# Kernel optimization log

Hardware: AMD Instinct MI355X
Metric: run time of the kernel (lower is better)

## Reference

```python
import jax, jax.numpy as jnp
import numpy as np

NUM_HEADS = 12
PRUNE_THRESHOLD = 0.5  # deterministic stand-in for torch.rand(1).item() seed_


def setup_inputs() -> dict:
    key = jax.random.key(0)
    ks = jax.random.split(key, 7)
    B, f, w, W, D = 4, 16, 8, 128, 768
    Bn = B * f * w
    return {
        "x": jax.random.normal(ks[0], (Bn, W, D), dtype=jnp.float32),
        "qkv_w": jax.random.normal(ks[1], (3 * D, D), dtype=jnp.float32) * (D ** -0.5),
        "qkv_b": jax.random.normal(ks[2], (3 * D,), dtype=jnp.float32) * 0.01,
        "proj_w": jax.random.normal(ks[3], (D, D), dtype=jnp.float32) * (D ** -0.5),
        "proj_b": jax.random.normal(ks[4], (D,), dtype=jnp.float32) * 0.01,
        "edge_bias": jax.random.uniform(ks[5], (1, NUM_HEADS, W, W), dtype=jnp.float32),
        "mask": jax.random.uniform(ks[6], (f * w, W, W), dtype=jnp.float32),
        "B": B,
        "f": f,
        "w": w,
    }


def reference(x, qkv_w, qkv_b, proj_w, proj_b, edge_bias, mask, B, f, w):
    Bn, W, D = x.shape              # Bn = B*f*w windows, W = tokens per window
    H = NUM_HEADS
    hd = D // H
    scale = hd ** -0.5

    qkv = x @ qkv_w.T + qkv_b                                   # [Bn, W, 3D]
    qkv = qkv.reshape(Bn, W, 3, H, hd).transpose(2, 0, 3, 1, 4)  # [3, Bn, H, W, hd]
    q, k, v = qkv[0] * scale, qkv[1], qkv[2]

    attn = jnp.einsum('bhqd,bhkd->bhqk', q, k)                  # [Bn, H, W, W]

    # stochastic softmax-threshold pruning (training branch), detached mask
    probs = jax.nn.softmax(attn, axis=-1)
    keep = jnp.where(probs > PRUNE_THRESHOLD, 0.0, 1.0)
    attn = attn * jax.lax.stop_gradient(keep)

    attn5 = attn.reshape(B, f * w, H, W, W)
    attn5 = attn5 * mask[None, :, None, :, :]                   # mask: [f*w, W, W]
    attn5 = attn5 * edge_bias[:, None]                          # edge_bias: [1, H, W, W]
    attn = attn5.reshape(Bn, H, W, W)

    attn = jnp.where(attn == 0, jnp.float32(-10000.0), attn)
    attn = jax.nn.softmax(attn, axis=-1)

    out = jnp.einsum('bhqk,bhkd->bhqd', attn, v)                # [Bn, H, W, hd]
    out = out.transpose(0, 2, 1, 3).reshape(Bn, W, D)
    return out @ proj_w.T + proj_b
```

## Files before the change

kernel.cpp:

```cpp
#include <hip/hip_runtime.h>

#define NW 512
#define WT 128
#define DM 768
#define NH 12

typedef __attribute__((ext_vector_type(8))) short bf16x8;
typedef __attribute__((ext_vector_type(4))) float f32x4;
typedef __attribute__((ext_vector_type(4))) unsigned int u32x4;

#define W1CH 12288
#define WS_W1 ((size_t)NH * 24 * W1CH)
#define PWCHUNK 49152
#define WS_W2 ((size_t)24 * PWCHUNK)

__device__ __forceinline__ unsigned short bf_rne(float v) {
  unsigned u = __float_as_uint(v);
  unsigned r = u + 0x7fffu + ((u >> 16) & 1u);
  return (unsigned short)(r >> 16);
}
__device__ __forceinline__ void bf_split(float v, unsigned short& hi, unsigned short& lo) {
  hi = bf_rne(v);
  float hf = __uint_as_float(((unsigned)hi) << 16);
  lo = bf_rne(v - hf);
}

__device__ __forceinline__ unsigned cvt_pk_bf16(float a, float b) {
  unsigned r;
  asm("v_cvt_pk_bf16_f32 %0, %1, %2" : "=v"(r) : "v"(a), "v"(b));
  return r;
}
__device__ __forceinline__ unsigned short bf_rne_fast(float v) {
  return (unsigned short)cvt_pk_bf16(v, v);
}
__device__ __forceinline__ void bf_split_fast(float v, unsigned short& hi, unsigned short& lo) {
  unsigned hp = cvt_pk_bf16(v, v);
  float hf = __uint_as_float(hp << 16);
  lo = (unsigned short)cvt_pk_bf16(v - hf, v - hf);
  hi = (unsigned short)hp;
}

__device__ __forceinline__ void split8(float4 v0, float4 v1, bf16x8& hi, bf16x8& lo) {
  float f[8] = {v0.x, v0.y, v0.z, v0.w, v1.x, v1.y, v1.z, v1.w};
  u32x4 hu, lu;
#pragma unroll
  for (int i = 0; i < 4; ++i) {
    float e0 = f[2 * i], e1 = f[2 * i + 1];
    unsigned hp = cvt_pk_bf16(e0, e1);
    float h0 = __uint_as_float(hp << 16);
    float h1 = __uint_as_float(hp & 0xffff0000u);
    lu[i] = cvt_pk_bf16(e0 - h0, e1 - h1);
    hu[i] = hp;
  }
  hi = __builtin_bit_cast(bf16x8, hu);
  lo = __builtin_bit_cast(bf16x8, lu);
}

__device__ __forceinline__ void gl_lds16(const void* g, void* l) {
  __builtin_amdgcn_global_load_lds(
      (const __attribute__((address_space(1))) void*)g,
      (__attribute__((address_space(3))) void*)l, 16, 0, 0);
}

__global__ __launch_bounds__(256) void split_w_kernel(
    const float* __restrict__ qkv_w, unsigned char* __restrict__ wsW)
{
  int id = blockIdx.x * 256 + threadIdx.x;
  int c4 = id & 7;
  int j  = (id >> 3) % 192;
  int hc = (id >> 3) / 192;
  int c  = hc % 24;
  int h  = hc / 24;
  int sec = j >> 6, d = j & 63;
  const float* src = qkv_w + (size_t)(sec * DM + h * 64 + d) * DM + c * 32 + c4 * 4;
  float4 v = *(const float4*)src;
  uint2 hv;
  hv.x = (unsigned)bf_rne(v.x) | ((unsigned)bf_rne(v.y) << 16);
  hv.y = (unsigned)bf_rne(v.z) | ((unsigned)bf_rne(v.w) << 16);
  int byte = j * 64 + (((c4 >> 1) ^ ((j >> 1) & 3)) << 4) + ((c4 & 1) << 3);
  *(uint2*)(wsW + (size_t)hc * W1CH + byte) = hv;
}

__global__ __launch_bounds__(256) void split_pw_kernel(
    const float* __restrict__ pw, unsigned char* __restrict__ wsP)
{
  int id = blockIdx.x * 256 + threadIdx.x;
  int c4 = id & 7;
  int n  = (id >> 3) % 768;
  int c  = (id >> 3) / 768;
  float4 v = *(const float4*)(pw + (size_t)n * DM + c * 32 + c4 * 4);
  uint2 hv;
  hv.x = (unsigned)bf_rne(v.x) | ((unsigned)bf_rne(v.y) << 16);
  hv.y = (unsigned)bf_rne(v.z) | ((unsigned)bf_rne(v.w) << 16);
  int byte = n * 64 + (((c4 >> 1) ^ ((n >> 1) & 3)) << 4) + ((c4 & 1) << 3);
  *(uint2*)(wsP + (size_t)c * PWCHUNK + byte) = hv;
}

#define QH_OFF 0
#define QL_OFF 16384
#define KH_OFF 32768
#define KL_OFF 49152
#define VT_OFF 65536
#define EX_OFF 49152
#define P_OFF  0

__global__ __launch_bounds__(512, 4) void attn_kernel_pre(
    const float* __restrict__ x, const unsigned char* __restrict__ wimg,
    const float* __restrict__ qkv_b, const float* __restrict__ edge_bias,
    const float* __restrict__ mask, float* __restrict__ out)
{
  __shared__ __align__(16) unsigned char smem[81920];
  const int t = threadIdx.x;
  const int lane = t & 63;
  const int w = t >> 6;
  const int g = lane >> 4;
  const int ln = lane & 15;
  const int wm = w & 3;
  const int wn = w >> 2;

  const int orig = blockIdx.x;
  const int wg = (orig & 7) * 768 + (orig >> 3);
  const int h = wg % 12;
  const int bn = wg / 12;

  const float* xw = x + (size_t)bn * (WT * DM);
  const unsigned char* whead = wimg + (size_t)h * (24 * W1CH);

  f32x4 acc[2][6];
#pragma unroll
  for (int i = 0; i < 2; ++i)
#pragma unroll
    for (int j = 0; j < 6; ++j) acc[i][j] = (f32x4){0.f, 0.f, 0.f, 0.f};

  const int exr = wm * 32 + (lane & 31);
  const int exs = wn * 2 + (lane >> 5);
  const float* xptr = xw + (size_t)exr * DM + wn * 16 + (lane >> 5) * 8;
  const int ex_w_hi = exr * 128 + ((exs ^ (exr & 7)) << 4);
  const int ex_w_lo = exr * 128 + (((exs + 4) ^ (exr & 7)) << 4);
  int ex_r_h[2], ex_r_l[2];
#pragma unroll
  for (int sm = 0; sm < 2; ++sm) {
    int rr = wm * 32 + sm * 16 + ln;
    ex_r_h[sm] = rr * 128 + ((g ^ (rr & 7)) << 4);
    ex_r_l[sm] = rr * 128 + (((g + 4) ^ (rr & 7)) << 4);
  }

  {
    gl_lds16(whead + t * 16, smem + t * 16);
    if (t < 256) gl_lds16(whead + 8192 + t * 16, smem + 8192 + t * 16);
  }
  __builtin_amdgcn_sched_barrier(0);
  float4 xa = *(const float4*)xptr;
  float4 xb = *(const float4*)(xptr + 4);
  __builtin_amdgcn_sched_barrier(0);

  for (int c = 0; c < 24; ++c) {
    float4 na, nb;
    if (c < 23) {
      na = *(const float4*)(xptr + (c + 1) * 32);
      nb = *(const float4*)(xptr + (c + 1) * 32 + 4);
    }
    __builtin_amdgcn_sched_barrier(0);
    bf16x8 xh8, xl8;
    split8(xa, xb, xh8, xl8);
    unsigned char* exb = smem + EX_OFF + (c & 1) * 16384;
    *(bf16x8*)(exb + ex_w_hi) = xh8;
    *(bf16x8*)(exb + ex_w_lo) = xl8;
    __builtin_amdgcn_sched_barrier(0);
    if (c < 23) asm volatile("s_waitcnt vmcnt(2)" ::: "memory");
    else        asm volatile("s_waitcnt vmcnt(0)" ::: "memory");
    asm volatile("s_waitcnt lgkmcnt(0)" ::: "memory");
    __builtin_amdgcn_s_barrier();
    __builtin_amdgcn_sched_barrier(0);
    if (c < 23) {
      const unsigned char* src = whead + (size_t)(c + 1) * W1CH;
      unsigned char* dst = smem + ((c + 1) & 1) * W1CH;
      gl_lds16(src + t * 16, dst + t * 16);
      if (t < 256) gl_lds16(src + 8192 + t * 16, dst + 8192 + t * 16);
    }
    __builtin_amdgcn_sched_barrier(0);
    const unsigned char* WH = smem + (c & 1) * W1CH;
    bf16x8 ah0 = *(const bf16x8*)(exb + ex_r_h[0]);
    bf16x8 al0 = *(const bf16x8*)(exb + ex_r_l[0]);
    bf16x8 ah1 = *(const bf16x8*)(exb + ex_r_h[1]);
    bf16x8 al1 = *(const bf16x8*)(exb + ex_r_l[1]);
    __builtin_amdgcn_s_setprio(1);
#pragma unroll
    for (int ns = 0; ns < 6; ++ns) {
      int j = (ns * 2 + wn) * 16 + ln;
      int sw = j * 64 + ((g ^ ((j >> 1) & 3)) << 4);
      bf16x8 bh = *(const bf16x8*)(WH + sw);
      acc[0][ns] = __builtin_amdgcn_mfma_f32_16x16x32_bf16(ah0, bh, acc[0][ns], 0, 0, 0);
      acc[1][ns] = __builtin_amdgcn_mfma_f32_16x16x32_bf16(ah1, bh, acc[1][ns], 0, 0, 0);
      if (ns < 4) {
        acc[0][ns] = __builtin_amdgcn_mfma_f32_16x16x32_bf16(al0, bh, acc[0][ns], 0, 0, 0);
        acc[1][ns] = __builtin_amdgcn_mfma_f32_16x16x32_bf16(al1, bh, acc[1][ns], 0, 0, 0);
      }
    }
    __builtin_amdgcn_s_setprio(0);
    xa = na; xb = nb;
  }
  __syncthreads();

#pragma unroll
  for (int ns = 0; ns < 6; ++ns) {
    int cc = (ns * 2 + wn) * 16 + ln;
    int sec = cc >> 6, dd = cc & 63;
    float bias = qkv_b[sec * DM + h * 64 + dd];
#pragma unroll
    for (int sm = 0; sm < 2; ++sm) {
#pragma unroll
      for (int r = 0; r < 4; ++r) {
        int m = wm * 32 + sm * 16 + 4 * g + r;
        float val = acc[sm][ns][r] + bias;
        if (cc < 64) {
          val *= 0.125f;
          unsigned short hi, lo; bf_split_fast(val, hi, lo);
          int byte = m * 128 + (((dd >> 3) ^ (m & 7)) << 4) + ((dd & 7) << 1);
          *(unsigned short*)(smem + QH_OFF + byte) = hi;
          *(unsigned short*)(smem + QL_OFF + byte) = lo;
        } else if (cc < 128) {
          unsigned short hi, lo; bf_split_fast(val, hi, lo);
          int byte = m * 128 + (((dd >> 3) ^ (m & 7)) << 4) + ((dd & 7) << 1);
          *(unsigned short*)(smem + KH_OFF + byte) = hi;
          *(unsigned short*)(smem + KL_OFF + byte) = lo;
        } else {
          int byte = dd * 256 + ((((m >> 3) ^ (dd & 15))) << 4) + ((m & 7) << 1);
          *(unsigned short*)(smem + VT_OFF + byte) = bf_rne_fast(val);
        }
      }
    }
  }
  __syncthreads();

  const int mB = w * 16;
  f32x4 s2[8];
#pragma unroll
  for (int ns = 0; ns < 8; ++ns) s2[ns] = (f32x4){0.f, 0.f, 0.f, 0.f};
#pragma unroll
  for (int ks = 0; ks < 2; ++ks) {
    int arow = mB + ln;
    int abyte = arow * 128 + (((ks * 4 + g) ^ (arow & 7)) << 4);
    bf16x8 qh = *(const bf16x8*)(smem + QH_OFF + abyte);
    bf16x8 ql = *(const bf16x8*)(smem + QL_OFF + abyte);
#pragma unroll
    for (int ns = 0; ns < 8; ++ns) {
      int brow = ns * 16 + ln;
      int bbyte = brow * 128 + (((ks * 4 + g) ^ (brow & 7)) << 4);
      bf16x8 kh = *(const bf16x8*)(smem + KH_OFF + bbyte);
      bf16x8 kl = *(const bf16x8*)(smem + KL_OFF + bbyte);
      s2[ns] = __builtin_amdgcn_mfma_f32_16x16x32_bf16(qh, kh, s2[ns], 0, 0, 0);
      s2[ns] = __builtin_amdgcn_mfma_f32_16x16x32_bf16(qh, kl, s2[ns], 0, 0, 0);
      s2[ns] = __builtin_amdgcn_mfma_f32_16x16x32_bf16(ql, kh, s2[ns], 0, 0, 0);
    }
  }
  __syncthreads();

  const float* mk = mask + (size_t)(bn & 127) * (WT * WT);
  const float* eb = edge_bias + (size_t)h * (WT * WT);
#pragma unroll
  for (int r = 0; r < 4; ++r) {
    int m = mB + 4 * g + r;
    float sv[8];
#pragma unroll
    for (int ns = 0; ns < 8; ++ns) sv[ns] = s2[ns][r];
    float m1 = sv[0];
#pragma unroll
    for (int ns = 1; ns < 8; ++ns) m1 = fmaxf(m1, sv[ns]);
#pragma unroll
    for (int off = 1; off < 16; off <<= 1) m1 = fmaxf(m1, __shfl_xor(m1, off, 64));
    float e[8], sum1 = 0.f;
#pragma unroll
    for (int ns = 0; ns < 8; ++ns) { e[ns] = __expf(sv[ns] - m1); sum1 += e[ns]; }
#pragma unroll
    for (int off = 1; off < 16; off <<= 1) sum1 += __shfl_xor(sum1, off, 64);
    float thr = 0.5f * sum1;
    float tv[8];
#pragma unroll
    for (int ns = 0; ns < 8; ++ns) {
      int col = ns * 16 + ln;
      float mkv = mk[m * WT + col];
      float ebv = eb[m * WT + col];
      float keep = (e[ns] > thr) ? 0.f : 1.f;
      float val = sv[ns] * keep * mkv * ebv;
      tv[ns] = (val == 0.f) ? -10000.f : val;
    }
    float m2 = tv[0];
#pragma unroll
    for (int ns = 1; ns < 8; ++ns) m2 = fmaxf(m2, tv[ns]);
#pragma unroll
    for (int off = 1; off < 16; off <<= 1) m2 = fmaxf(m2, __shfl_xor(m2, off, 64));
    float e2[8], sum2 = 0.f;
#pragma unroll
    for (int ns = 0; ns < 8; ++ns) { e2[ns] = __expf(tv[ns] - m2); sum2 += e2[ns]; }
#pragma unroll
    for (int off = 1; off < 16; off <<= 1) sum2 += __shfl_xor(sum2, off, 64);
    float inv = 1.f / sum2;
#pragma unroll
    for (int ns = 0; ns < 8; ++ns)
      *(unsigned short*)(smem + P_OFF + m * 272 + (ns * 16 + ln) * 2) = bf_rne_fast(e2[ns] * inv);
  }
  __syncthreads();

  f32x4 o4[4];
#pragma unroll
  for (int ns = 0; ns < 4; ++ns) o4[ns] = (f32x4){0.f, 0.f, 0.f, 0.f};
#pragma unroll
  for (int ks = 0; ks < 4; ++ks) {
    bf16x8 pa = *(const bf16x8*)(smem + P_OFF + (mB + ln) * 272 + ks * 64 + g * 16);
#pragma unroll
    for (int ns = 0; ns < 4; ++ns) {
      int d = ns * 16 + ln;
      bf16x8 vb = *(const bf16x8*)(smem + VT_OFF + d * 256 + (((ks * 4 + g) ^ (d & 15)) << 4));
      o4[ns] = __builtin_amdgcn_mfma_f32_16x16x32_bf16(pa, vb, o4[ns], 0, 0, 0);
    }
  }
#pragma unroll
  for (int ns = 0; ns < 4; ++ns)
#pragma unroll
    for (int r = 0; r < 4; ++r)
      out[(size_t)bn * (WT * DM) + (size_t)(mB + 4 * g + r) * DM + h * 64 + ns * 16 + ln] = o4[ns][r];
}

#define PAOFF 147456

__global__ __launch_bounds__(512) void proj_kernel_pre(
    const float* src, const unsigned char* __restrict__ wimg,
    const float* __restrict__ pb, float* dst)
{
  __shared__ __align__(16) unsigned char smem[159744];
  const int t = threadIdx.x;
  const int lane = t & 63;
  const int w = t >> 6;
  const int g = lane >> 4;
  const int ln = lane & 15;
  const int wm = w & 1;
  const int wn = w >> 1;

  const int orig = blockIdx.x;
  const int wg = (orig & 7) * 128 + (orig >> 3);
  const size_t row0 = (size_t)wg * 64;

  const int ar = t >> 3, ac4 = t & 7;
  const float* asrc = src + (row0 + ar) * DM + ac4 * 4;
  const int abyte = ar * 64 + (((ac4 >> 1) ^ ((ar >> 1) & 3)) << 4) + ((ac4 & 1) << 3);
  int afh[2];
#pragma unroll
  for (int sm = 0; sm < 2; ++sm) {
    int rr = wm * 32 + sm * 16 + ln;
    afh[sm] = rr * 64 + ((g ^ ((rr >> 1) & 3)) << 4);
  }

  {
    const unsigned char* sW = wimg + t * 16;
#pragma unroll
    for (int i = 0; i < 6; ++i) gl_lds16(sW + i * 8192, smem + t * 16 + i * 8192);
    const unsigned char* sW1 = wimg + PWCHUNK + t * 16;
#pragma unroll
    for (int i = 0; i < 6; ++i) gl_lds16(sW1 + i * 8192, smem + PWCHUNK + t * 16 + i * 8192);
  }
  __builtin_amdgcn_sched_barrier(0);
  float4 a0 = *(const float4*)asrc;
  float4 a1 = *(const float4*)(asrc + 32);
  {
    uint2 wv; wv.x = cvt_pk_bf16(a0.x, a0.y); wv.y = cvt_pk_bf16(a0.z, a0.w);
    *(uint2*)(smem + PAOFF + abyte) = wv;
  }
  __builtin_amdgcn_sched_barrier(0);

  f32x4 acc[2][12];
#pragma unroll
  for (int i = 0; i < 2; ++i)
#pragma unroll
    for (int j = 0; j < 12; ++j) acc[i][j] = (f32x4){0.f, 0.f, 0.f, 0.f};

  for (int c = 0; c < 24; ++c) {
    float4 a2;
    if (c < 22) a2 = *(const float4*)(asrc + (c + 2) * 32);
    __builtin_amdgcn_sched_barrier(0);
    if (c < 23) {
      uint2 wv; wv.x = cvt_pk_bf16(a1.x, a1.y); wv.y = cvt_pk_bf16(a1.z, a1.w);
      *(uint2*)(smem + PAOFF + ((c + 1) % 3) * 4096 + abyte) = wv;
    }
    __builtin_amdgcn_sched_barrier(0);
    if (c < 22)       asm volatile("s_waitcnt vmcnt(8)" ::: "memory");
    else if (c == 22) asm volatile("s_waitcnt vmcnt(7)" ::: "memory");
    else              asm volatile("s_waitcnt vmcnt(0)" ::: "memory");
    asm volatile("s_waitcnt lgkmcnt(0)" ::: "memory");
    __builtin_amdgcn_s_barrier();
    __builtin_amdgcn_sched_barrier(0);
    if (c < 22) {
      const unsigned char* sW = wimg + (size_t)(c + 2) * PWCHUNK + t * 16;
      unsigned char* dW = smem + ((c + 2) % 3) * PWCHUNK + t * 16;
#pragma unroll
      for (int i = 0; i < 6; ++i) gl_lds16(sW + i * 8192, dW + i * 8192);
    }
    __builtin_amdgcn_sched_barrier(0);
    const unsigned char* WB = smem + (c % 3) * PWCHUNK;
    const unsigned char* AB = smem + PAOFF + (c % 3) * 4096;
    bf16x8 af0 = *(const bf16x8*)(AB + afh[0]);
    bf16x8 af1 = *(const bf16x8*)(AB + afh[1]);
    __builtin_amdgcn_s_setprio(1);
#pragma unroll
    for (int ns = 0; ns < 12; ++ns) {
      int n = wn * 192 + ns * 16 + ln;
      bf16x8 bfrag = *(const bf16x8*)(WB + n * 64 + ((g ^ ((n >> 1) & 3)) << 4));
      acc[0][ns] = __builtin_amdgcn_mfma_f32_16x16x32_bf16(af0, bfrag, acc[0][ns], 0, 0, 0);
      acc[1][ns] = __builtin_amdgcn_mfma_f32_16x16x32_bf16(af1, bfrag, acc[1][ns], 0, 0, 0);
    }
    __builtin_amdgcn_s_setprio(0);
    a1 = a2;
  }

#pragma unroll
  for (int ns = 0; ns < 12; ++ns) {
    int col = wn * 192 + ns * 16 + ln;
    float pbv = pb[col];
#pragma unroll
    for (int sm = 0; sm < 2; ++sm)
#pragma unroll
      for (int r = 0; r < 4; ++r)
        dst[(row0 + wm * 32 + sm * 16 + 4 * g + r) * DM + col] = acc[sm][ns][r] + pbv;
  }
}

__global__ __launch_bounds__(512, 2) void attn_kernel_fb(
    const float* __restrict__ x, const float* __restrict__ qkv_w,
    const float* __restrict__ qkv_b, const float* __restrict__ edge_bias,
    const float* __restrict__ mask, float* __restrict__ out)
{
  __shared__ __align__(16) unsigned char smem[98304];
  const int t = threadIdx.x;
  const int lane = t & 63;
  const int w = t >> 6;
  const int g = lane >> 4;
  const int ln = lane & 15;
  const int wm = w & 3;
  const int wn = w >> 2;

  const int orig = blockIdx.x;
  const int wg = (orig & 7) * 768 + (orig >> 3);
  const int h = wg % 12;
  const int bn = wg / 12;

  const float* xw = x + (size_t)bn * (WT * DM);

  f32x4 acc[2][6];
#pragma unroll
  for (int i = 0; i < 2; ++i)
#pragma unroll
    for (int j = 0; j < 6; ++j) acc[i][j] = (f32x4){0.f, 0.f, 0.f, 0.f};

  float4 wreg[6], xreg[8];
#pragma unroll
  for (int q = 0; q < 6; ++q) {
    int fid = q * 512 + t;
    int j = fid >> 4, c4 = fid & 15;
    int sec = j >> 6, d = j & 63;
    wreg[q] = *(const float4*)(qkv_w + (size_t)(sec * DM + h * 64 + d) * DM + c4 * 4);
  }

  for (int c = 0; c < 12; ++c) {
    const int kc = c * 64;
#pragma unroll
    for (int sm = 0; sm < 2; ++sm)
#pragma unroll
      for (int ks = 0; ks < 2; ++ks) {
        int row = wm * 32 + sm * 16 + ln;
        const float* p = xw + (size_t)row * DM + kc + ks * 32 + g * 8;
        xreg[(sm * 2 + ks) * 2 + 0] = *(const float4*)p;
        xreg[(sm * 2 + ks) * 2 + 1] = *(const float4*)(p + 4);
      }
    unsigned char* WH = smem + (c & 1) * 49152;
    unsigned char* WL = WH + 24576;
#pragma unroll
    for (int q = 0; q < 6; ++q) {
      int fid = q * 512 + t;
      int j = fid >> 4, c4 = fid & 15;
      int byte = j * 128 + ((((c4 >> 1) ^ (j & 7))) << 4) + ((c4 & 1) << 3);
      float4 v = wreg[q];
      unsigned short h0, h1, h2, h3, l0, l1, l2, l3;
      bf_split(v.x, h0, l0); bf_split(v.y, h1, l1);
      bf_split(v.z, h2, l2); bf_split(v.w, h3, l3);
      uint2 hv, lv;
      hv.x = (unsigned)h0 | ((unsigned)h1 << 16); hv.y = (unsigned)h2 | ((unsigned)h3 << 16);
      lv.x = (unsigned)l0 | ((unsigned)l1 << 16); lv.y = (unsigned)l2 | ((unsigned)l3 << 16);
      *(uint2*)(WH + byte) = hv;
      *(uint2*)(WL + byte) = lv;
    }
    if (c < 11) {
#pragma unroll
      for (int q = 0; q < 6; ++q) {
        int fid = q * 512 + t;
        int j = fid >> 4, c4 = fid & 15;
        int sec = j >> 6, d = j & 63;
        wreg[q] = *(const float4*)(qkv_w + (size_t)(sec * DM + h * 64 + d) * DM + kc + 64 + c4 * 4);
      }
    }
    __syncthreads();
#pragma unroll
    for (int ks = 0; ks < 2; ++ks) {
      bf16x8 ah[2], al[2];
#pragma unroll
      for (int sm = 0; sm < 2; ++sm)
        split8(xreg[(sm * 2 + ks) * 2 + 0], xreg[(sm * 2 + ks) * 2 + 1], ah[sm], al[sm]);
#pragma unroll
      for (int ns = 0; ns < 6; ++ns) {
        int j = wn * 96 + ns * 16 + ln;
        int sw = j * 128 + (((ks * 4 + g) ^ (j & 7)) << 4);
        bf16x8 bh = *(const bf16x8*)(WH + sw);
        bf16x8 bl = *(const bf16x8*)(WL + sw);
#pragma unroll
        for (int sm = 0; sm < 2; ++sm) {
          acc[sm][ns] = __builtin_amdgcn_mfma_f32_16x16x32_bf16(ah[sm], bh, acc[sm][ns], 0, 0, 0);
          acc[sm][ns] = __builtin_amdgcn_mfma_f32_16x16x32_bf16(ah[sm], bl, acc[sm][ns], 0, 0, 0);
          acc[sm][ns] = __builtin_amdgcn_mfma_f32_16x16x32_bf16(al[sm], bh, acc[sm][ns], 0, 0, 0);
        }
      }
    }
  }
  __syncthreads();

#pragma unroll
  for (int sm = 0; sm < 2; ++sm)
#pragma unroll
    for (int ns = 0; ns < 6; ++ns) {
      int cc = wn * 96 + ns * 16 + ln;
      int sec = cc >> 6, dd = cc & 63;
      float bias = qkv_b[sec * DM + h * 64 + dd];
#pragma unroll
      for (int r = 0; r < 4; ++r) {
        int m = wm * 32 + sm * 16 + 4 * g + r;
        float val = acc[sm][ns][r] + bias;
        if (cc < 64) {
          val *= 0.125f;
          unsigned short hi, lo; bf_split(val, hi, lo);
          int byte = m * 128 + ((((dd >> 3) ^ (m & 7))) << 4) + ((dd & 7) << 1);
          *(unsigned short*)(smem + QH_OFF + byte) = hi;
          *(unsigned short*)(smem + QL_OFF + byte) = lo;
        } else if (cc < 128) {
          unsigned short hi, lo; bf_split(val, hi, lo);
          int byte = m * 128 + ((((dd >> 3) ^ (m & 7))) << 4) + ((dd & 7) << 1);
          *(unsigned short*)(smem + KH_OFF + byte) = hi;
          *(unsigned short*)(smem + KL_OFF + byte) = lo;
        } else {
          *(unsigned short*)(smem + VT_OFF + dd * 272 + m * 2) = bf_rne(val);
        }
      }
    }
  __syncthreads();

  const int mB = w * 16;
  f32x4 s2[8];
#pragma unroll
  for (int ns = 0; ns < 8; ++ns) s2[ns] = (f32x4){0.f, 0.f, 0.f, 0.f};
#pragma unroll
  for (int ks = 0; ks < 2; ++ks) {
    int arow = mB + ln;
    int abyte = arow * 128 + (((ks * 4 + g) ^ (arow & 7)) << 4);
    bf16x8 qh = *(const bf16x8*)(smem + QH_OFF + abyte);
    bf16x8 ql = *(const bf16x8*)(smem + QL_OFF + abyte);
#pragma unroll
    for (int ns = 0; ns < 8; ++ns) {
      int brow = ns * 16 + ln;
      int bbyte = brow * 128 + (((ks * 4 + g) ^ (brow & 7)) << 4);
      bf16x8 kh = *(const bf16x8*)(smem + KH_OFF + bbyte);
      bf16x8 kl = *(const bf16x8*)(smem + KL_OFF + bbyte);
      s2[ns] = __builtin_amdgcn_mfma_f32_16x16x32_bf16(qh, kh, s2[ns], 0, 0, 0);
      s2[ns] = __builtin_amdgcn_mfma_f32_16x16x32_bf16(qh, kl, s2[ns], 0, 0, 0);
      s2[ns] = __builtin_amdgcn_mfma_f32_16x16x32_bf16(ql, kh, s2[ns], 0, 0, 0);
    }
  }
  __syncthreads();

  const float* mk = mask + (size_t)(bn & 127) * (WT * WT);
  const float* eb = edge_bias + (size_t)h * (WT * WT);
#pragma unroll
  for (int r = 0; r < 4; ++r) {
    int m = mB + 4 * g + r;
    float sv[8];
#pragma unroll
    for (int ns = 0; ns < 8; ++ns) sv[ns] = s2[ns][r];
    float m1 = sv[0];
#pragma unroll
    for (int ns = 1; ns < 8; ++ns) m1 = fmaxf(m1, sv[ns]);
#pragma unroll
    for (int off = 1; off < 16; off <<= 1) m1 = fmaxf(m1, __shfl_xor(m1, off, 64));
    float e[8], sum1 = 0.f;
#pragma unroll
    for (int ns = 0; ns < 8; ++ns) { e[ns] = __expf(sv[ns] - m1); sum1 += e[ns]; }
#pragma unroll
    for (int off = 1; off < 16; off <<= 1) sum1 += __shfl_xor(sum1, off, 64);
    float thr = 0.5f * sum1;
    float tv[8];
#pragma unroll
    for (int ns = 0; ns < 8; ++ns) {
      int col = ns * 16 + ln;
      float mkv = mk[m * WT + col];
      float ebv = eb[m * WT + col];
      float keep = (e[ns] > thr) ? 0.f : 1.f;
      float val = sv[ns] * keep * mkv * ebv;
      tv[ns] = (val == 0.f) ? -10000.f : val;
    }
    float m2 = tv[0];
#pragma unroll
    for (int ns = 1; ns < 8; ++ns) m2 = fmaxf(m2, tv[ns]);
#pragma unroll
    for (int off = 1; off < 16; off <<= 1) m2 = fmaxf(m2, __shfl_xor(m2, off, 64));
    float e2[8], sum2 = 0.f;
#pragma unroll
    for (int ns = 0; ns < 8; ++ns) { e2[ns] = __expf(tv[ns] - m2); sum2 += e2[ns]; }
#pragma unroll
    for (int off = 1; off < 16; off <<= 1) sum2 += __shfl_xor(sum2, off, 64);
    float inv = 1.f / sum2;
#pragma unroll
    for (int ns = 0; ns < 8; ++ns)
      *(unsigned short*)(smem + P_OFF + m * 272 + (ns * 16 + ln) * 2) = bf_rne(e2[ns] * inv);
  }
  __syncthreads();

  f32x4 o4[4];
#pragma unroll
  for (int ns = 0; ns < 4; ++ns) o4[ns] = (f32x4){0.f, 0.f, 0.f, 0.f};
#pragma unroll
  for (int ks = 0; ks < 4; ++ks) {
    bf16x8 pa = *(const bf16x8*)(smem + P_OFF + (mB + ln) * 272 + ks * 64 + g * 16);
#pragma unroll
    for (int ns = 0; ns < 4; ++ns) {
      bf16x8 vb = *(const bf16x8*)(smem + VT_OFF + (ns * 16 + ln) * 272 + ks * 64 + g * 16);
      o4[ns] = __builtin_amdgcn_mfma_f32_16x16x32_bf16(pa, vb, o4[ns], 0, 0, 0);
    }
  }
#pragma unroll
  for (int ns = 0; ns < 4; ++ns)
#pragma unroll
    for (int r = 0; r < 4; ++r)
      out[(size_t)bn * (WT * DM) + (size_t)(mB + 4 * g + r) * DM + h * 64 + ns * 16 + ln] = o4[ns][r];
}

#define PA_OFF 0
#define PW_OFF 98304

__global__ __launch_bounds__(512, 2) void proj_kernel_fb(
    const float* src, const float* __restrict__ pw,
    const float* __restrict__ pb, float* dst)
{
  __shared__ __align__(16) unsigned char smem[147456];
  const int t = threadIdx.x;
  const int lane = t & 63;
  const int w = t >> 6;
  const int g = lane >> 4;
  const int ln = lane & 15;
  const int wm = w & 1;
  const int wn = w >> 1;

  const int orig = blockIdx.x;
  const int wg = (orig & 7) * 128 + (orig >> 3);
  const size_t row0 = (size_t)wg * 64;

#pragma unroll
  for (int q = 0; q < 24; ++q) {
    int fid = q * 512 + t;
    int row = fid / 192, c4 = fid % 192;
    float4 v = *(const float4*)(src + (row0 + row) * DM + c4 * 4);
    int slot = c4 >> 1;
    int byte = row * 1536 + (((slot & ~7) | ((slot & 7) ^ (row & 7))) << 4) + ((c4 & 1) << 3);
    uint2 hv;
    hv.x = (unsigned)bf_rne(v.x) | ((unsigned)bf_rne(v.y) << 16);
    hv.y = (unsigned)bf_rne(v.z) | ((unsigned)bf_rne(v.w) << 16);
    *(uint2*)(smem + PA_OFF + byte) = hv;
  }

  f32x4 accp[2][12];
#pragma unroll
  for (int i = 0; i < 2; ++i)
#pragma unroll
    for (int j = 0; j < 12; ++j) accp[i][j] = (f32x4){0.f, 0.f, 0.f, 0.f};

  for (int c = 0; c < 24; ++c) {
    const int kc = c * 32;
    __syncthreads();
#pragma unroll
    for (int q = 0; q < 12; ++q) {
      int fid = q * 512 + t;
      int n = fid >> 3, c4 = fid & 7;
      float4 v = *(const float4*)(pw + (size_t)n * DM + kc + c4 * 4);
      int slot = (n & 1) * 4 + (c4 >> 1);
      int byte = (n >> 1) * 128 + ((slot ^ ((n >> 1) & 7)) << 4) + ((c4 & 1) << 3);
      uint2 hv;
      hv.x = (unsigned)bf_rne(v.x) | ((unsigned)bf_rne(v.y) << 16);
      hv.y = (unsigned)bf_rne(v.z) | ((unsigned)bf_rne(v.w) << 16);
      *(uint2*)(smem + PW_OFF + byte) = hv;
    }
    __syncthreads();
    bf16x8 af[2];
#pragma unroll
    for (int sm = 0; sm < 2; ++sm) {
      int row = wm * 32 + sm * 16 + ln;
      int slot = (kc >> 3) + g;
      int byte = row * 1536 + (((slot & ~7) | ((slot & 7) ^ (row & 7))) << 4);
      af[sm] = *(const bf16x8*)(smem + PA_OFF + byte);
    }
#pragma unroll
    for (int j = 0; j < 12; ++j) {
      int n = (wn * 12 + j) * 16 + ln;
      int slot = (n & 1) * 4 + g;
      bf16x8 bf_ = *(const bf16x8*)(smem + PW_OFF + (n >> 1) * 128 + ((slot ^ ((n >> 1) & 7)) << 4));
#pragma unroll
      for (int sm = 0; sm < 2; ++sm)
        accp[sm][j] = __builtin_amdgcn_mfma_f32_16x16x32_bf16(af[sm], bf_, accp[sm][j], 0, 0, 0);
    }
  }

#pragma unroll
  for (int j = 0; j < 12; ++j) {
    int col = (wn * 12 + j) * 16 + ln;
    float pbv = pb[col];
#pragma unroll
    for (int sm = 0; sm < 2; ++sm)
#pragma unroll
      for (int r = 0; r < 4; ++r)
        dst[(row0 + wm * 32 + sm * 16 + 4 * g + r) * DM + col] = accp[sm][j][r] + pbv;
  }
}

extern "C" void kernel_launch(void* const* d_in, const int* in_sizes, int n_in,
                              void* d_out, int out_size, void* d_ws, size_t ws_size,
                              hipStream_t stream) {
  const float* x         = (const float*)d_in[0];
  const float* qkv_w     = (const float*)d_in[1];
  const float* qkv_b     = (const float*)d_in[2];
  const float* proj_w    = (const float*)d_in[3];
  const float* proj_b    = (const float*)d_in[4];
  const float* edge_bias = (const float*)d_in[5];
  const float* mask      = (const float*)d_in[6];
  float* out = (float*)d_out;

  const bool p1 = (d_ws != nullptr) && (ws_size >= WS_W1);
  const bool p2 = (d_ws != nullptr) && (ws_size >= WS_W1 + WS_W2);
  unsigned char* wsW = (unsigned char*)d_ws;
  unsigned char* wsP = wsW + WS_W1;

  if (p1) {
    split_w_kernel<<<1728, 256, 0, stream>>>(qkv_w, wsW);
  }
  if (p2) {
    split_pw_kernel<<<576, 256, 0, stream>>>(proj_w, wsP);
  }
  if (p1) {
    attn_kernel_pre<<<NW * NH, 512, 0, stream>>>(x, wsW, qkv_b, edge_bias, mask, out);
  } else {
    attn_kernel_fb<<<NW * NH, 512, 0, stream>>>(x, qkv_w, qkv_b, edge_bias, mask, out);
  }
  if (p2) {
    proj_kernel_pre<<<1024, 512, 0, stream>>>(out, wsP, proj_b, out);
  } else {
    proj_kernel_fb<<<1024, 512, 0, stream>>>(out, proj_w, proj_b, out);
  }
}
```

Before: 704.2 us.

## Split fused attention into batched QKV-projection and attention kernels via workspace

```diff
diff --git a/kernel.cpp b/kernel.cpp
--- a/kernel.cpp
+++ b/kernel.cpp
@@ -13,6 +13,7 @@
 #define WS_W1 ((size_t)NH * 24 * W1CH)
 #define PWCHUNK 49152
 #define WS_W2 ((size_t)24 * PWCHUNK)
+#define IMG_SZ 81920
 
 __device__ __forceinline__ unsigned short bf_rne(float v) {
   unsigned u = __float_as_uint(v);
@@ -60,6 +61,11 @@
   __builtin_amdgcn_global_load_lds(
       (const __attribute__((address_space(1))) void*)g,
       (__attribute__((address_space(3))) void*)l, 16, 0, 0);
+}
+__device__ __forceinline__ void gl_lds4(const void* g, void* l) {
+  __builtin_amdgcn_global_load_lds(
+      (const __attribute__((address_space(1))) void*)g,
+      (__attribute__((address_space(3))) void*)l, 4, 0, 0);
 }
 
 __global__ __launch_bounds__(256) void split_w_kernel(
@@ -103,6 +109,242 @@
 #define VT_OFF 65536
 #define EX_OFF 49152
 #define P_OFF  0
+
+__global__ __launch_bounds__(512, 2) void qkv2_kernel(
+    const float* __restrict__ x, const unsigned char* __restrict__ wimg,
+    const float* __restrict__ qkv_b, unsigned char* __restrict__ att, int p0)
+{
+  __shared__ __align__(16) unsigned char smem[24576];
+  const int t = threadIdx.x;
+  const int lane = t & 63;
+  const int w = t >> 6;
+  const int g = lane >> 4;
+  const int ln = lane & 15;
+  const int wm = w & 3;
+  const int win = w >> 2;
+
+  const int nwg = gridDim.x;
+  const int orig = blockIdx.x;
+  const int wg = (orig & 7) * (nwg >> 3) + (orig >> 3);
+  const int h = wg % 12;
+  const int lp = wg / 12;
+  const int bn = 2 * (p0 + lp) + win;
+
+  const float* xw = x + (size_t)bn * (WT * DM);
+  const unsigned char* whead = wimg + (size_t)h * (24 * W1CH);
+  unsigned char* img = att + ((size_t)(lp * 2 + win) * NH + h) * IMG_SZ;
+
+  f32x4 acc[2][12];
+#pragma unroll
+  for (int i = 0; i < 2; ++i)
+#pragma unroll
+    for (int j = 0; j < 12; ++j) acc[i][j] = (f32x4){0.f, 0.f, 0.f, 0.f};
+
+  const float* xp0 = xw + (size_t)(wm * 32 + ln) * DM + g * 8;
+  const float* xp1 = xp0 + (size_t)16 * DM;
+
+  auto stageW = [&](int c, int buf) {
+    const unsigned char* s = whead + (size_t)c * W1CH + w * 1536;
+    unsigned char* d = smem + buf * W1CH + w * 1536;
+    gl_lds16(s + lane * 16, d + lane * 16);
+    gl_lds4(s + 1024 + lane * 4, d + 1024 + lane * 4);
+    gl_lds4(s + 1280 + lane * 4, d + 1280 + lane * 4);
+  };
+
+  stageW(0, 0);
+  __builtin_amdgcn_sched_barrier(0);
+  float4 xc0 = *(const float4*)xp0;
+  float4 xc1 = *(const float4*)(xp0 + 4);
+  float4 xc2 = *(const float4*)xp1;
+  float4 xc3 = *(const float4*)(xp1 + 4);
+  float4 xn0 = *(const float4*)(xp0 + 32);
+  float4 xn1 = *(const float4*)(xp0 + 36);
+  float4 xn2 = *(const float4*)(xp1 + 32);
+  float4 xn3 = *(const float4*)(xp1 + 36);
+  __builtin_amdgcn_sched_barrier(0);
+
+  for (int c = 0; c < 24; ++c) {
+    int cn = (c + 2 < 24 ? c + 2 : 23) * 32;
+    float4 nf0 = *(const float4*)(xp0 + cn);
+    float4 nf1 = *(const float4*)(xp0 + cn + 4);
+    float4 nf2 = *(const float4*)(xp1 + cn);
+    float4 nf3 = *(const float4*)(xp1 + cn + 4);
+    __builtin_amdgcn_sched_barrier(0);
+    bf16x8 ah0, al0, ah1, al1;
+    split8(xc0, xc1, ah0, al0);
+    split8(xc2, xc3, ah1, al1);
+    __builtin_amdgcn_sched_barrier(0);
+    asm volatile("s_waitcnt vmcnt(4)" ::: "memory");
+    __builtin_amdgcn_s_barrier();
+    __builtin_amdgcn_sched_barrier(0);
+    {
+      int cw = (c + 1 < 24 ? c + 1 : 23);
+      stageW(cw, (c + 1) & 1);
+    }
+    __builtin_amdgcn_sched_barrier(0);
+    const unsigned char* WH = smem + (c & 1) * W1CH;
+    __builtin_amdgcn_s_setprio(1);
+#pragma unroll
+    for (int ns = 0; ns < 12; ++ns) {
+      int j = ns * 16 + ln;
+      int sw = j * 64 + ((g ^ ((j >> 1) & 3)) << 4);
+      bf16x8 bh = *(const bf16x8*)(WH + sw);
+      acc[0][ns] = __builtin_amdgcn_mfma_f32_16x16x32_bf16(ah0, bh, acc[0][ns], 0, 0, 0);
+      acc[1][ns] = __builtin_amdgcn_mfma_f32_16x16x32_bf16(ah1, bh, acc[1][ns], 0, 0, 0);
+      if (ns < 8) {
+        acc[0][ns] = __builtin_amdgcn_mfma_f32_16x16x32_bf16(al0, bh, acc[0][ns], 0, 0, 0);
+        acc[1][ns] = __builtin_amdgcn_mfma_f32_16x16x32_bf16(al1, bh, acc[1][ns], 0, 0, 0);
+      }
+    }
+    __builtin_amdgcn_s_setprio(0);
+    xc0 = xn0; xc1 = xn1; xc2 = xn2; xc3 = xn3;
+    xn0 = nf0; xn1 = nf1; xn2 = nf2; xn3 = nf3;
+  }
+
+#pragma unroll
+  for (int ns = 0; ns < 12; ++ns) {
+    int cc = ns * 16 + ln;
+    int sec = cc >> 6, dd = cc & 63;
+    float bias = qkv_b[sec * DM + h * 64 + dd];
+#pragma unroll
+    for (int sm = 0; sm < 2; ++sm) {
+#pragma unroll
+      for (int r = 0; r < 4; ++r) {
+        int m = wm * 32 + sm * 16 + 4 * g + r;
+        float val = acc[sm][ns][r] + bias;
+        if (cc < 64) {
+          val *= 0.125f;
+          unsigned short hi, lo; bf_split_fast(val, hi, lo);
+          int byte = m * 128 + (((dd >> 3) ^ (m & 7)) << 4) + ((dd & 7) << 1);
+          *(unsigned short*)(img + QH_OFF + byte) = hi;
+          *(unsigned short*)(img + QL_OFF + byte) = lo;
+        } else if (cc < 128) {
+          unsigned short hi, lo; bf_split_fast(val, hi, lo);
+          int byte = m * 128 + (((dd >> 3) ^ (m & 7)) << 4) + ((dd & 7) << 1);
+          *(unsigned short*)(img + KH_OFF + byte) = hi;
+          *(unsigned short*)(img + KL_OFF + byte) = lo;
+        } else {
+          int byte = dd * 256 + ((((m >> 3) ^ (dd & 15))) << 4) + ((m & 7) << 1);
+          *(unsigned short*)(img + VT_OFF + byte) = bf_rne_fast(val);
+        }
+      }
+    }
+  }
+}
+
+__global__ __launch_bounds__(512, 4) void attn2_kernel(
+    const unsigned char* __restrict__ att, const float* __restrict__ edge_bias,
+    const float* __restrict__ mask, float* __restrict__ out, int w0)
+{
+  __shared__ __align__(16) unsigned char smem[81920];
+  const int t = threadIdx.x;
+  const int lane = t & 63;
+  const int w = t >> 6;
+  const int g = lane >> 4;
+  const int ln = lane & 15;
+
+  const int nwg = gridDim.x;
+  const int orig = blockIdx.x;
+  const int wg = (orig & 7) * (nwg >> 3) + (orig >> 3);
+  const int h = wg % 12;
+  const int lw = wg / 12;
+  const int bn = w0 + lw;
+
+  const unsigned char* img = att + ((size_t)lw * NH + h) * IMG_SZ;
+#pragma unroll
+  for (int i = 0; i < 10; ++i)
+    gl_lds16(img + i * 8192 + t * 16, smem + i * 8192 + t * 16);
+  asm volatile("s_waitcnt vmcnt(0)" ::: "memory");
+  __syncthreads();
+
+  const int mB = w * 16;
+  f32x4 s2[8];
+#pragma unroll
+  for (int ns = 0; ns < 8; ++ns) s2[ns] = (f32x4){0.f, 0.f, 0.f, 0.f};
+#pragma unroll
+  for (int ks = 0; ks < 2; ++ks) {
+    int arow = mB + ln;
+    int abyte = arow * 128 + (((ks * 4 + g) ^ (arow & 7)) << 4);
+    bf16x8 qh = *(const bf16x8*)(smem + QH_OFF + abyte);
+    bf16x8 ql = *(const bf16x8*)(smem + QL_OFF + abyte);
+#pragma unroll
+    for (int ns = 0; ns < 8; ++ns) {
+      int brow = ns * 16 + ln;
+      int bbyte = brow * 128 + (((ks * 4 + g) ^ (brow & 7)) << 4);
+      bf16x8 kh = *(const bf16x8*)(smem + KH_OFF + bbyte);
+      bf16x8 kl = *(const bf16x8*)(smem + KL_OFF + bbyte);
+      s2[ns] = __builtin_amdgcn_mfma_f32_16x16x32_bf16(qh, kh, s2[ns], 0, 0, 0);
+      s2[ns] = __builtin_amdgcn_mfma_f32_16x16x32_bf16(qh, kl, s2[ns], 0, 0, 0);
+      s2[ns] = __builtin_amdgcn_mfma_f32_16x16x32_bf16(ql, kh, s2[ns], 0, 0, 0);
+    }
+  }
+  __syncthreads();
+
+  const float* mk = mask + (size_t)(bn & 127) * (WT * WT);
+  const float* eb = edge_bias + (size_t)h * (WT * WT);
+#pragma unroll
+  for (int r = 0; r < 4; ++r) {
+    int m = mB + 4 * g + r;
+    float sv[8];
+#pragma unroll
+    for (int ns = 0; ns < 8; ++ns) sv[ns] = s2[ns][r];
+    float m1 = sv[0];
+#pragma unroll
+    for (int ns = 1; ns < 8; ++ns) m1 = fmaxf(m1, sv[ns]);
+#pragma unroll
+    for (int off = 1; off < 16; off <<= 1) m1 = fmaxf(m1, __shfl_xor(m1, off, 64));
+    float e[8], sum1 = 0.f;
+#pragma unroll
+    for (int ns = 0; ns < 8; ++ns) { e[ns] = __expf(sv[ns] - m1); sum1 += e[ns]; }
+#pragma unroll
+    for (int off = 1; off < 16; off <<= 1) sum1 += __shfl_xor(sum1, off, 64);
+    float thr = 0.5f * sum1;
+    float tv[8];
+#pragma unroll
+    for (int ns = 0; ns < 8; ++ns) {
+      int col = ns * 16 + ln;
+      float mkv = mk[m * WT + col];
+      float ebv = eb[m * WT + col];
+      float keep = (e[ns] > thr) ? 0.f : 1.f;
+      float val = sv[ns] * keep * mkv * ebv;
+      tv[ns] = (val == 0.f) ? -10000.f : val;
+    }
+    float m2 = tv[0];
+#pragma unroll
+    for (int ns = 1; ns < 8; ++ns) m2 = fmaxf(m2, tv[ns]);
+#pragma unroll
+    for (int off = 1; off < 16; off <<= 1) m2 = fmaxf(m2, __shfl_xor(m2, off, 64));
+    float e2[8], sum2 = 0.f;
+#pragma unroll
+    for (int ns = 0; ns < 8; ++ns) { e2[ns] = __expf(tv[ns] - m2); sum2 += e2[ns]; }
+#pragma unroll
+    for (int off = 1; off < 16; off <<= 1) sum2 += __shfl_xor(sum2, off, 64);
+    float inv = 1.f / sum2;
+#pragma unroll
+    for (int ns = 0; ns < 8; ++ns)
+      *(unsigned short*)(smem + P_OFF + m * 272 + (ns * 16 + ln) * 2) = bf_rne_fast(e2[ns] * inv);
+  }
+  __syncthreads();
+
+  f32x4 o4[4];
+#pragma unroll
+  for (int ns = 0; ns < 4; ++ns) o4[ns] = (f32x4){0.f, 0.f, 0.f, 0.f};
+#pragma unroll
+  for (int ks = 0; ks < 4; ++ks) {
+    bf16x8 pa = *(const bf16x8*)(smem + P_OFF + (mB + ln) * 272 + ks * 64 + g * 16);
+#pragma unroll
+    for (int ns = 0; ns < 4; ++ns) {
+      int d = ns * 16 + ln;
+      bf16x8 vb = *(const bf16x8*)(smem + VT_OFF + d * 256 + (((ks * 4 + g) ^ (d & 15)) << 4));
+      o4[ns] = __builtin_amdgcn_mfma_f32_16x16x32_bf16(pa, vb, o4[ns], 0, 0, 0);
+    }
+  }
+#pragma unroll
+  for (int ns = 0; ns < 4; ++ns)
+#pragma unroll
+    for (int r = 0; r < 4; ++r)
+      out[(size_t)bn * (WT * DM) + (size_t)(mB + 4 * g + r) * DM + h * 64 + ns * 16 + ln] = o4[ns][r];
+}
 
 __global__ __launch_bounds__(512, 4) void attn_kernel_pre(
     const float* __restrict__ x, const unsigned char* __restrict__ wimg,
@@ -424,6 +666,92 @@
   }
 }
 
+#define PA_OFF 0
+#define PW_OFF 98304
+
+__global__ __launch_bounds__(512, 2) void proj_kernel_fb(
+    const float* src, const float* __restrict__ pw,
+    const float* __restrict__ pb, float* dst)
+{
+  __shared__ __align__(16) unsigned char smem[147456];
+  const int t = threadIdx.x;
+  const int lane = t & 63;
+  const int w = t >> 6;
+  const int g = lane >> 4;
+  const int ln = lane & 15;
+  const int wm = w & 1;
+  const int wn = w >> 1;
+
+  const int orig = blockIdx.x;
+  const int wg = (orig & 7) * 128 + (orig >> 3);
+  const size_t row0 = (size_t)wg * 64;
+
+#pragma unroll
+  for (int q = 0; q < 24; ++q) {
+    int fid = q * 512 + t;
+    int row = fid / 192, c4 = fid % 192;
+    float4 v = *(const float4*)(src + (row0 + row) * DM + c4 * 4);
+    int slot = c4 >> 1;
+    int byte = row * 1536 + (((slot & ~7) | ((slot & 7) ^ (row & 7))) << 4) + ((c4 & 1) << 3);
+    uint2 hv;
+    hv.x = (unsigned)bf_rne(v.x) | ((unsigned)bf_rne(v.y) << 16);
+    hv.y = (unsigned)bf_rne(v.z) | ((unsigned)bf_rne(v.w) << 16);
+    *(uint2*)(smem + PA_OFF + byte) = hv;
+  }
+
+  f32x4 accp[2][12];
+#pragma unroll
+  for (int i = 0; i < 2; ++i)
+#pragma unroll
+    for (int j = 0; j < 12; ++j) accp[i][j] = (f32x4){0.f, 0.f, 0.f, 0.f};
+
+  for (int c = 0; c < 24; ++c) {
+    const int kc = c * 32;
+    __syncthreads();
+#pragma unroll
+    for (int q = 0; q < 12; ++q) {
+      int fid = q * 512 + t;
+      int n = fid >> 3, c4 = fid & 7;
+      float4 v = *(const float4*)(pw + (size_t)n * DM + kc + c4 * 4);
+      int slot = (n & 1) * 4 + (c4 >> 1);
+      int byte = (n >> 1) * 128 + ((slot ^ ((n >> 1) & 7)) << 4) + ((c4 & 1) << 3);
+      uint2 hv;
+      hv.x = (unsigned)bf_rne(v.x) | ((unsigned)bf_rne(v.y) << 16);
+      hv.y = (unsigned)bf_rne(v.z) | ((unsigned)bf_rne(v.w) << 16);
+      *(uint2*)(smem + PW_OFF + byte) = hv;
+    }
+    __syncthreads();
+    bf16x8 af[2];
+#pragma unroll
+    for (int sm = 0; sm < 2; ++sm) {
+      int row = wm * 32 + sm * 16 + ln;
+      int slot = (kc >> 3) + g;
+      int byte = row * 1536 + (((slot & ~7) | ((slot & 7) ^ (row & 7))) << 4);
+      af[sm] = *(const bf16x8*)(smem + PA_OFF + byte);
+    }
+#pragma unroll
+    for (int j = 0; j < 12; ++j) {
+      int n = (wn * 12 + j) * 16 + ln;
+      int slot = (n & 1) * 4 + g;
+      bf16x8 bf_ = *(const bf16x8*)(smem + PW_OFF + (n >> 1) * 128 + ((slot ^ ((n >> 1) & 7)) << 4));
+#pragma unroll
+      for (int sm = 0; sm < 2; ++sm)
+        accp[sm][j] = __builtin_amdgcn_mfma_f32_16x16x32_bf16(af[sm], bf_, accp[sm][j], 0, 0, 0);
+    }
+  }
+
+#pragma unroll
+  for (int j = 0; j < 12; ++j) {
+    int col = (wn * 12 + j) * 16 + ln;
+    float pbv = pb[col];
+#pragma unroll
+    for (int sm = 0; sm < 2; ++sm)
+#pragma unroll
+      for (int r = 0; r < 4; ++r)
+        dst[(row0 + wm * 32 + sm * 16 + 4 * g + r) * DM + col] = accp[sm][j][r] + pbv;
+  }
+}
+
 __global__ __launch_bounds__(512, 2) void attn_kernel_fb(
     const float* __restrict__ x, const float* __restrict__ qkv_w,
     const float* __restrict__ qkv_b, const float* __restrict__ edge_bias,
@@ -638,92 +966,6 @@
       out[(size_t)bn * (WT * DM) + (size_t)(mB + 4 * g + r) * DM + h * 64 + ns * 16 + ln] = o4[ns][r];
 }
 
-#define PA_OFF 0
-#define PW_OFF 98304
-
-__global__ __launch_bounds__(512, 2) void proj_kernel_fb(
-    const float* src, const float* __restrict__ pw,
-    const float* __restrict__ pb, float* dst)
-{
-  __shared__ __align__(16) unsigned char smem[147456];
-  const int t = threadIdx.x;
-  const int lane = t & 63;
-  const int w = t >> 6;
-  const int g = lane >> 4;
-  const int ln = lane & 15;
-  const int wm = w & 1;
-  const int wn = w >> 1;
-
-  const int orig = blockIdx.x;
-  const int wg = (orig & 7) * 128 + (orig >> 3);
-  const size_t row0 = (size_t)wg * 64;
-
-#pragma unroll
-  for (int q = 0; q < 24; ++q) {
-    int fid = q * 512 + t;
-    int row = fid / 192, c4 = fid % 192;
-    float4 v = *(const float4*)(src + (row0 + row) * DM + c4 * 4);
-    int slot = c4 >> 1;
-    int byte = row * 1536 + (((slot & ~7) | ((slot & 7) ^ (row & 7))) << 4) + ((c4 & 1) << 3);
-    uint2 hv;
-    hv.x = (unsigned)bf_rne(v.x) | ((unsigned)bf_rne(v.y) << 16);
-    hv.y = (unsigned)bf_rne(v.z) | ((unsigned)bf_rne(v.w) << 16);
-    *(uint2*)(smem + PA_OFF + byte) = hv;
-  }
-
-  f32x4 accp[2][12];
-#pragma unroll
-  for (int i = 0; i < 2; ++i)
-#pragma unroll
-    for (int j = 0; j < 12; ++j) accp[i][j] = (f32x4){0.f, 0.f, 0.f, 0.f};
-
-  for (int c = 0; c < 24; ++c) {
-    const int kc = c * 32;
-    __syncthreads();
-#pragma unroll
-    for (int q = 0; q < 12; ++q) {
-      int fid = q * 512 + t;
-      int n = fid >> 3, c4 = fid & 7;
-      float4 v = *(const float4*)(pw + (size_t)n * DM + kc + c4 * 4);
-      int slot = (n & 1) * 4 + (c4 >> 1);
-      int byte = (n >> 1) * 128 + ((slot ^ ((n >> 1) & 7)) << 4) + ((c4 & 1) << 3);
-      uint2 hv;
-      hv.x = (unsigned)bf_rne(v.x) | ((unsigned)bf_rne(v.y) << 16);
-      hv.y = (unsigned)bf_rne(v.z) | ((unsigned)bf_rne(v.w) << 16);
-      *(uint2*)(smem + PW_OFF + byte) = hv;
-    }
-    __syncthreads();
-    bf16x8 af[2];
-#pragma unroll
-    for (int sm = 0; sm < 2; ++sm) {
-      int row = wm * 32 + sm * 16 + ln;
-      int slot = (kc >> 3) + g;
-      int byte = row * 1536 + (((slot & ~7) | ((slot & 7) ^ (row & 7))) << 4);
-      af[sm] = *(const bf16x8*)(smem + PA_OFF + byte);
-    }
-#pragma unroll
-    for (int j = 0; j < 12; ++j) {
-      int n = (wn * 12 + j) * 16 + ln;
-      int slot = (n & 1) * 4 + g;
-      bf16x8 bf_ = *(const bf16x8*)(smem + PW_OFF + (n >> 1) * 128 + ((slot ^ ((n >> 1) & 7)) << 4));
-#pragma unroll
-      for (int sm = 0; sm < 2; ++sm)
-        accp[sm][j] = __builtin_amdgcn_mfma_f32_16x16x32_bf16(af[sm], bf_, accp[sm][j], 0, 0, 0);
-    }
-  }
-
-#pragma unroll
-  for (int j = 0; j < 12; ++j) {
-    int col = (wn * 12 + j) * 16 + ln;
-    float pbv = pb[col];
-#pragma unroll
-    for (int sm = 0; sm < 2; ++sm)
-#pragma unroll
-      for (int r = 0; r < 4; ++r)
-        dst[(row0 + wm * 32 + sm * 16 + 4 * g + r) * DM + col] = accp[sm][j][r] + pbv;
-  }
-}
-
 extern "C" void kernel_launch(void* const* d_in, const int* in_sizes, int n_in,
                               void* d_out, int out_size, void* d_ws, size_t ws_size,
                               hipStream_t stream) {
@@ -740,18 +982,28 @@
   const bool p2 = (d_ws != nullptr) && (ws_size >= WS_W1 + WS_W2);
   unsigned char* wsW = (unsigned char*)d_ws;
   unsigned char* wsP = wsW + WS_W1;
-
-  if (p1) {
-    split_w_kernel<<<1728, 256, 0, stream>>>(qkv_w, wsW);
-  }
-  if (p2) {
-    split_pw_kernel<<<576, 256, 0, stream>>>(proj_w, wsP);
-  }
-  if (p1) {
+  unsigned char* wsA = wsP + WS_W2;
+
+  const size_t base = WS_W1 + WS_W2;
+  int nb = 0;
+  if (p2 && ws_size >= base + (size_t)64 * 24 * IMG_SZ)      nb = 4;
+  else if (p2 && ws_size >= base + (size_t)32 * 24 * IMG_SZ) nb = 8;
+
+  if (p1) split_w_kernel<<<1728, 256, 0, stream>>>(qkv_w, wsW);
+  if (p2) split_pw_kernel<<<576, 256, 0, stream>>>(proj_w, wsP);
+
+  if (nb) {
+    const int pb = 256 / nb;
+    for (int b = 0; b < nb; ++b) {
+      qkv2_kernel<<<pb * 12, 512, 0, stream>>>(x, wsW, qkv_b, wsA, b * pb);
+      attn2_kernel<<<pb * 24, 512, 0, stream>>>(wsA, edge_bias, mask, out, b * pb * 2);
+    }
+  } else if (p1) {
     attn_kernel_pre<<<NW * NH, 512, 0, stream>>>(x, wsW, qkv_b, edge_bias, mask, out);
   } else {
     attn_kernel_fb<<<NW * NH, 512, 0, stream>>>(x, qkv_w, qkv_b, edge_bias, mask, out);
   }
+
   if (p2) {
     proj_kernel_pre<<<1024, 512, 0, stream>>>(out, wsP, proj_b, out);
   } else {
```

Result: slower. 900.6 us (+27.9%).
